# Optimization experiments

Measured on AMD Instinct MI355X. Metric: run time of the kernel, lower is better.

Reference implementation:

```python
import jax, jax.numpy as jnp
import numpy as np

B_SZ, SEQ, D_IN, D_ST, D_OUT = 16, 8192, 128, 128, 128


def setup_inputs() -> dict:
    key = jax.random.key(0)
    ku, ka, kb, kc, kd = jax.random.split(key, 5)
    u = jax.random.normal(ku, (B_SZ, SEQ, D_IN), dtype=jnp.float32)
    # A scaled to spectral radius ~0.9 so the long recurrence stays stable
    A = jax.random.normal(ka, (D_ST, D_ST), dtype=jnp.float32) * (0.9 / np.sqrt(D_ST))
    B = jax.random.normal(kb, (D_ST, D_IN), dtype=jnp.float32) * (1.0 / np.sqrt(D_IN))
    C = jax.random.normal(kc, (D_OUT, D_ST), dtype=jnp.float32) * (1.0 / np.sqrt(D_ST))
    D = jax.random.normal(kd, (D_OUT, D_IN), dtype=jnp.float32) * (1.0 / np.sqrt(D_IN))
    return {"u": u, "A": A, "B": B, "C": C, "D": D}


def reference(u, A, B, C, D):
    # x_t = x_{t-1} A^T + u_t B^T ; y_t = x_t C^T + u_t D^T ; x_0 = 0
    batch = u.shape[0]
    state0 = jnp.zeros((batch, A.shape[0]), dtype=u.dtype)

    def step(state, u_t):  # state: [B, S_dim], u_t: [B, D_in]
        new_state = state @ A.T + u_t @ B.T
        y = new_state @ C.T + u_t @ D.T
        return new_state, y

    u_t_first = jnp.swapaxes(u, 0, 1)  # [SEQ, B, D_in]
    _, ys = jax.lax.scan(step, state0, u_t_first)
    return jnp.swapaxes(ys, 0, 1)  # [B, SEQ, D_out]
```

## Files before the change

kernel.cpp:

```cpp
#include <hip/hip_runtime.h>


#define SEQ 8192
#define BS  16
#define DD  128
#define CL  16
#define NC  512
#define GRP 16
#define NG  32

typedef __bf16 bf16t;
typedef __bf16 bf16x8 __attribute__((ext_vector_type(8)));
typedef __bf16 bf16x4 __attribute__((ext_vector_type(4)));
typedef float  f32x4  __attribute__((ext_vector_type(4)));

#define MFMA(a,b,c) __builtin_amdgcn_mfma_f32_16x16x32_bf16(a,b,c,0,0,0)

__device__ __forceinline__ int swz(int b, int j) { return j ^ ((b & 7) << 3); }

struct Frag  { bf16x8 h[4]; bf16x8 l[4]; };
struct FragH { bf16x8 h[4]; };

__device__ __forceinline__ void load_frag_T(const float* __restrict__ src, int lane, int w, Frag& f) {
    int n  = (w << 4) + (lane & 15);
    int kb = ((lane >> 4) & 3) << 3;
#pragma unroll
    for (int q = 0; q < 4; q++) {
        const float* p = src + n * DD + (q << 5) + kb;
#pragma unroll
        for (int e = 0; e < 8; e++) {
            float v = p[e];
            bf16t hh = (bf16t)v;
            f.h[q][e] = hh;
            f.l[q][e] = (bf16t)(v - (float)hh);
        }
    }
}

__device__ __forceinline__ void load_frag_T_h(const float* __restrict__ src, int lane, int w, FragH& f) {
    int n  = (w << 4) + (lane & 15);
    int kb = ((lane >> 4) & 3) << 3;
#pragma unroll
    for (int q = 0; q < 4; q++) {
        const float* p = src + n * DD + (q << 5) + kb;
#pragma unroll
        for (int e = 0; e < 8; e++) f.h[q][e] = (bf16t)p[e];
    }
}

__device__ __forceinline__ void load_frag_N(const float* __restrict__ src, int lane, int w, Frag& f) {
    int n  = (w << 4) + (lane & 15);
    int kb = ((lane >> 4) & 3) << 3;
#pragma unroll
    for (int q = 0; q < 4; q++) {
#pragma unroll
        for (int e = 0; e < 8; e++) {
            float v = src[((q << 5) + kb + e) * DD + n];
            bf16t hh = (bf16t)v;
            f.h[q][e] = hh;
            f.l[q][e] = (bf16t)(v - (float)hh);
        }
    }
}

__device__ __forceinline__ bf16x8 afrag(const bf16t* __restrict__ X, int lane, int q) {
    int b  = lane & 15;
    int j0 = (q << 5) + (((lane >> 4) & 3) << 3);
    return *(const bf16x8*)(X + b * DD + swz(b, j0));
}

__device__ __forceinline__ void put_state(bf16t* __restrict__ H, bf16t* __restrict__ L,
                                          int lane, int w, f32x4 acc) {
    int n = (w << 4) + (lane & 15);
#pragma unroll
    for (int r = 0; r < 4; r++) {
        int b = (((lane >> 4) & 3) << 2) + r;
        float v = acc[r];
        bf16t hh = (bf16t)v;
        H[b * DD + swz(b, n)] = hh;
        L[b * DD + swz(b, n)] = (bf16t)(v - (float)hh);
    }
}

__device__ __forceinline__ void stage_rows(const float* __restrict__ src, long rs,
                                           bf16t* __restrict__ H, bf16t* __restrict__ L, int tid) {
    int b  = tid >> 5;
    int j0 = (tid & 31) << 2;
    float4 v = *(const float4*)(src + (long)b * rs + j0);
    float vv[4] = { v.x, v.y, v.z, v.w };
    bf16x4 h, l;
#pragma unroll
    for (int e = 0; e < 4; e++) {
        bf16t hh = (bf16t)vv[e];
        h[e] = hh;
        l[e] = (bf16t)(vv[e] - (float)hh);
    }
    *(bf16x4*)(H + b * DD + swz(b, j0)) = h;
    *(bf16x4*)(L + b * DD + swz(b, j0)) = l;
}

__device__ __forceinline__ void write_u_h(bf16t* __restrict__ H, int b_, int j0_, float4 v) {
    float vv[4] = { v.x, v.y, v.z, v.w };
    bf16x4 h;
#pragma unroll
    for (int e = 0; e < 4; e++) h[e] = (bf16t)vv[e];
    *(bf16x4*)(H + b_ * DD + swz(b_, j0_)) = h;
}

__device__ __forceinline__ f32x4 load_accfrag(const float* __restrict__ src, int lane, int w) {
    int n = (w << 4) + (lane & 15);
    f32x4 a;
#pragma unroll
    for (int r = 0; r < 4; r++) {
        int b = (((lane >> 4) & 3) << 2) + r;
        a[r] = src[b * DD + n];
    }
    return a;
}

__device__ __forceinline__ void store_accfrag(float* __restrict__ dst, int lane, int w,
                                              f32x4 a, long rs) {
    int n = (w << 4) + (lane & 15);
#pragma unroll
    for (int r = 0; r < 4; r++) {
        int b = (((lane >> 4) & 3) << 2) + r;
        dst[(long)b * rs + n] = a[r];
    }
}

__global__ __launch_bounds__(128) void k_prepGH(const float* __restrict__ A,
                                                const float* __restrict__ B,
                                                const float* __restrict__ C,
                                                const float* __restrict__ D,
                                                float* __restrict__ Gm, float* __restrict__ Hm) {
    int sel = blockIdx.x >> 7, r = blockIdx.x & 127, j = threadIdx.x;
    const float* R = sel ? B : A;
    float s = 0.f;
#pragma unroll 8
    for (int m = 0; m < 128; m++) s = fmaf(C[r * 128 + m], R[m * 128 + j], s);
    if (sel) Hm[r * 128 + j] = s + D[r * 128 + j];
    else     Gm[r * 128 + j] = s;
}

__global__ __launch_bounds__(512, 4) void k_chunk(const float* __restrict__ u,
                                                  const float* __restrict__ A,
                                                  const float* __restrict__ Bm,
                                                  float* __restrict__ E,
                                                  float* __restrict__ P) {
    __shared__ __align__(16) bf16t Xh[2][BS * DD], Xl[2][BS * DD];
    __shared__ __align__(16) bf16t Uh[2][BS * DD];
    int tid = threadIdx.x, lane = tid & 63, w = tid >> 6;
    bool ident = blockIdx.x < 8;
    int g2 = blockIdx.x, c = blockIdx.x - 8;

    Frag fA; FragH fB;
    load_frag_T(A, lane, w, fA);
    if (!ident) load_frag_T_h(Bm, lane, w, fB);

    for (int i = tid; i < BS * DD; i += 512) {
        int b = i >> 7, j = swz(b, i & 127);
        Xh[0][i] = (bf16t)((ident && j == g2 * 16 + b) ? 1.f : 0.f);
        Xl[0][i] = (bf16t)0.f;
    }
    const float* ubase = u + (long)c * CL * DD;
    int b_ = tid >> 5, j0_ = (tid & 31) << 2;
    if (!ident) {
        float4 v0 = *(const float4*)(ubase + (long)b_ * SEQ * DD + j0_);
        write_u_h(Uh[0], b_, j0_, v0);
    }
    __syncthreads();

    int p = 0;
    f32x4 acc = {0.f, 0.f, 0.f, 0.f};
    for (int i = 0; i < CL; i++) {
        float4 un = {0, 0, 0, 0};
        if (!ident && i + 1 < CL)
            un = *(const float4*)(ubase + (long)b_ * SEQ * DD + (i + 1) * DD + j0_);
        f32x4 ax = {0,0,0,0}, ax2 = {0,0,0,0};
#pragma unroll
        for (int q = 0; q < 4; q++) {
            bf16x8 xh = afrag(Xh[p], lane, q), xl = afrag(Xl[p], lane, q);
            ax  = MFMA(xh, fA.h[q], ax);
            ax2 = MFMA(xl, fA.h[q], ax2);
            ax2 = MFMA(xh, fA.l[q], ax2);
            if (!ident) {
                bf16x8 uh = afrag(Uh[i & 1], lane, q);
                ax = MFMA(uh, fB.h[q], ax);
            }
        }
        acc = ax + ax2;
        if (i + 1 < CL) {
            put_state(Xh[p ^ 1], Xl[p ^ 1], lane, w, acc);
            if (!ident) write_u_h(Uh[(i + 1) & 1], b_, j0_, un);
            __syncthreads();
            p ^= 1;
        }
    }
    if (!ident) store_accfrag(E + (long)c * BS * DD, lane, w, acc, DD);
    else        store_accfrag(P + (long)g2 * 16 * DD, lane, w, acc, DD);
}

__global__ __launch_bounds__(512) void k_group(const float* __restrict__ E,
                                               const float* __restrict__ P,
                                               float* __restrict__ E2,
                                               float* __restrict__ Pg) {
    __shared__ __align__(16) bf16t Xh[2][BS * DD], Xl[2][BS * DD];
    int tid = threadIdx.x, lane = tid & 63, w = tid >> 6;
    bool ident = blockIdx.x >= NG;
    int g2 = blockIdx.x - NG;
    Frag fP;
    load_frag_N(P, lane, w, fP);
    for (int i = tid; i < BS * DD; i += 512) {
        int b = i >> 7, j = swz(b, i & 127);
        Xh[0][i] = (bf16t)((ident && j == g2 * 16 + b) ? 1.f : 0.f);
        Xl[0][i] = (bf16t)0.f;
    }
    __syncthreads();
    int p = 0, g = blockIdx.x;
    f32x4 acc = {0.f, 0.f, 0.f, 0.f};
    for (int r = 0; r < GRP; r++) {
        f32x4 a1 = {0.f,0.f,0.f,0.f}, a2 = {0.f,0.f,0.f,0.f};
        if (!ident) a1 = load_accfrag(E + (long)(g * GRP + r) * BS * DD, lane, w);
#pragma unroll
        for (int q = 0; q < 4; q++) {
            bf16x8 xh = afrag(Xh[p], lane, q), xl = afrag(Xl[p], lane, q);
            a1 = MFMA(xh, fP.h[q], a1);
            a2 = MFMA(xl, fP.h[q], a2);
            a1 = MFMA(xh, fP.l[q], a1);
        }
        acc = a1 + a2;
        if (r + 1 < GRP) {
            put_state(Xh[p ^ 1], Xl[p ^ 1], lane, w, acc);
            __syncthreads();
            p ^= 1;
        }
    }
    if (!ident) store_accfrag(E2 + (long)g * BS * DD, lane, w, acc, DD);
    else        store_accfrag(Pg + (long)g2 * 16 * DD, lane, w, acc, DD);
}

__global__ __launch_bounds__(512) void k_top(const float* __restrict__ E2,
                                             const float* __restrict__ Pg,
                                             float* __restrict__ S2) {
    __shared__ __align__(16) bf16t Xh[2][BS * DD], Xl[2][BS * DD];
    int tid = threadIdx.x, lane = tid & 63, w = tid >> 6;
    Frag fP;
    load_frag_N(Pg, lane, w, fP);
    for (int i = tid; i < BS * DD; i += 512) {
        Xh[0][i] = (bf16t)0.f;
        Xl[0][i] = (bf16t)0.f;
    }
    __syncthreads();
    int p = 0;
    f32x4 T = {0.f, 0.f, 0.f, 0.f};
    f32x4 e2 = load_accfrag(E2, lane, w);
    for (int g = 0; g < NG; g++) {
        store_accfrag(S2 + (long)g * BS * DD, lane, w, T, DD);
        if (g + 1 == NG) break;
        f32x4 e2n = load_accfrag(E2 + (long)(g + 1) * BS * DD, lane, w);
        f32x4 a1 = e2, a2 = {0.f,0.f,0.f,0.f};
#pragma unroll
        for (int q = 0; q < 4; q++) {
            bf16x8 xh = afrag(Xh[p], lane, q), xl = afrag(Xl[p], lane, q);
            a1 = MFMA(xh, fP.h[q], a1);
            a2 = MFMA(xl, fP.h[q], a2);
            a1 = MFMA(xh, fP.l[q], a1);
        }
        T = a1 + a2;
        put_state(Xh[p ^ 1], Xl[p ^ 1], lane, w, T);
        __syncthreads();
        p ^= 1;
        e2 = e2n;
    }
}

__global__ __launch_bounds__(512) void k_fix(float* __restrict__ E,
                                             const float* __restrict__ P,
                                             const float* __restrict__ S2) {
    __shared__ __align__(16) bf16t Xh[2][BS * DD], Xl[2][BS * DD];
    int tid = threadIdx.x, lane = tid & 63, w = tid >> 6;
    int g = blockIdx.x;
    Frag fP;
    load_frag_N(P, lane, w, fP);
    stage_rows(S2 + (long)g * BS * DD, DD, Xh[0], Xl[0], tid);
    f32x4 T = load_accfrag(S2 + (long)g * BS * DD, lane, w);
    __syncthreads();
    int p = 0;
    for (int r = 0; r < GRP; r++) {
        long c = (long)(g * GRP + r) * BS * DD;
        if (r + 1 == GRP) { store_accfrag(E + c, lane, w, T, DD); break; }
        f32x4 a1 = load_accfrag(E + c, lane, w);
        store_accfrag(E + c, lane, w, T, DD);
        f32x4 a2 = {0.f,0.f,0.f,0.f};
#pragma unroll
        for (int q = 0; q < 4; q++) {
            bf16x8 xh = afrag(Xh[p], lane, q), xl = afrag(Xl[p], lane, q);
            a1 = MFMA(xh, fP.h[q], a1);
            a2 = MFMA(xl, fP.h[q], a2);
            a1 = MFMA(xh, fP.l[q], a1);
        }
        T = a1 + a2;
        put_state(Xh[p ^ 1], Xl[p ^ 1], lane, w, T);
        __syncthreads();
        p ^= 1;
    }
}

__global__ __launch_bounds__(512, 4) void k_main(const float* __restrict__ u,
                                                 const float* __restrict__ A,
                                                 const float* __restrict__ Bm,
                                                 const float* __restrict__ Gm,
                                                 const float* __restrict__ Hm,
                                                 const float* __restrict__ S,
                                                 float* __restrict__ out) {
    __shared__ __align__(16) bf16t Xh[2][BS * DD], Xl[2][BS * DD];
    __shared__ __align__(16) bf16t Uh[2][BS * DD];
    int tid = threadIdx.x, lane = tid & 63, w = tid >> 6;
    Frag fA; FragH fB, fG, fH;
    load_frag_T(A, lane, w, fA);
    load_frag_T_h(Bm, lane, w, fB);
    load_frag_T_h(Gm, lane, w, fG);
    load_frag_T_h(Hm, lane, w, fH);
    int c = blockIdx.x;
    const float* ubase = u + (long)c * CL * DD;
    int b_ = tid >> 5, j0_ = (tid & 31) << 2;
    stage_rows(S + (long)c * BS * DD, DD, Xh[0], Xl[0], tid);
    {
        float4 v0 = *(const float4*)(ubase + (long)b_ * SEQ * DD + j0_);
        write_u_h(Uh[0], b_, j0_, v0);
    }
    __syncthreads();
    int p = 0;
    for (int i = 0; i < CL; i++) {
        float4 un = {0, 0, 0, 0};
        if (i + 1 < CL)
            un = *(const float4*)(ubase + (long)b_ * SEQ * DD + (i + 1) * DD + j0_);
        f32x4 ax = {0,0,0,0}, ax2 = {0,0,0,0};
        f32x4 ay = {0,0,0,0}, ay2 = {0,0,0,0};
#pragma unroll
        for (int q = 0; q < 4; q++) {
            bf16x8 xh = afrag(Xh[p], lane, q), xl = afrag(Xl[p], lane, q);
            bf16x8 uh = afrag(Uh[i & 1], lane, q);
            ax  = MFMA(xh, fA.h[q], ax);
            ax  = MFMA(uh, fB.h[q], ax);
            ax2 = MFMA(xl, fA.h[q], ax2);
            ax2 = MFMA(xh, fA.l[q], ax2);
            ay  = MFMA(xh, fG.h[q], ay);
            ay  = MFMA(uh, fH.h[q], ay);
            ay2 = MFMA(xl, fG.h[q], ay2);
        }
        f32x4 xnew = ax + ax2;
        if (i + 1 < CL) {
            put_state(Xh[p ^ 1], Xl[p ^ 1], lane, w, xnew);
            write_u_h(Uh[(i + 1) & 1], b_, j0_, un);
        }
        f32x4 y = ay + ay2;
        store_accfrag(out + ((long)c * CL + i) * DD, lane, w, y, (long)SEQ * DD);
        if (i + 1 < CL) {
            __syncthreads();
            p ^= 1;
        }
    }
}

extern "C" void kernel_launch(void* const* d_in, const int* in_sizes, int n_in,
                              void* d_out, int out_size, void* d_ws, size_t ws_size,
                              hipStream_t stream) {
    (void)in_sizes; (void)n_in; (void)out_size; (void)ws_size;
    const float* u = (const float*)d_in[0];
    const float* A = (const float*)d_in[1];
    const float* B = (const float*)d_in[2];
    const float* C = (const float*)d_in[3];
    const float* D = (const float*)d_in[4];
    float* out = (float*)d_out;
    float* ws  = (float*)d_ws;
    float* Gm = ws;
    float* Hm = Gm + 16384;
    float* P  = Hm + 16384;
    float* Pg = P  + 16384;
    float* E  = Pg + 16384;
    float* E2 = E  + 1048576;
    float* S2 = E2 + 65536;
    dim3 blk(512);
    k_prepGH<<<256, 128, 0, stream>>>(A, B, C, D, Gm, Hm);
    k_chunk<<<NC + 8, blk, 0, stream>>>(u, A, B, E, P);
    k_group<<<NG + 8, blk, 0, stream>>>(E, P, E2, Pg);
    k_top  <<<1,      blk, 0, stream>>>(E2, Pg, S2);
    k_fix  <<<NG,     blk, 0, stream>>>(E, P, S2);
    k_main <<<NC,     blk, 0, stream>>>(u, A, B, Gm, Hm, E, out);
}
```

Before: 137.1 us.

## Replace sequential chunk scan with precomputed A-power kernel matmul and bf16 carries

Precomputes A^2, A^4, A^8, A^16 and the products A^k·B with small MFMA matmul kernels, packing them into one bf16 matrix. Each chunk's end-state contribution then becomes a single parallel GEMM over the 16 inputs instead of a 16-step dependent recurrence. Intermediate carries (E, E2, S2) are stored in bf16, and pass2 stages all chunk inputs into shared memory up front. Barriers use a lighter custom sequence. This adds four small serial prep launches and lowers the precision of the carried states.

Measured after the change: 256.8 us. 1.87x slower.

```diff
diff --git a/kernel.cpp b/kernel.cpp
--- a/kernel.cpp
+++ b/kernel.cpp
@@ -21,6 +21,12 @@
 struct Frag  { bf16x8 h[4]; bf16x8 l[4]; };
 struct FragH { bf16x8 h[4]; };
 
+__device__ __forceinline__ void step_barrier() {
+    asm volatile("s_waitcnt lgkmcnt(0)" ::: "memory");
+    __builtin_amdgcn_s_barrier();
+    __builtin_amdgcn_sched_barrier(0);
+}
+
 __device__ __forceinline__ void load_frag_T(const float* __restrict__ src, int lane, int w, Frag& f) {
     int n  = (w << 4) + (lane & 15);
     int kb = ((lane >> 4) & 3) << 3;
@@ -82,40 +88,36 @@
     }
 }
 
-__device__ __forceinline__ void stage_rows(const float* __restrict__ src, long rs,
-                                           bf16t* __restrict__ H, bf16t* __restrict__ L, int tid) {
+__device__ __forceinline__ void stage_rowsB(const bf16t* __restrict__ src,
+                                            bf16t* __restrict__ H, bf16t* __restrict__ L, int tid) {
     int b  = tid >> 5;
     int j0 = (tid & 31) << 2;
-    float4 v = *(const float4*)(src + (long)b * rs + j0);
-    float vv[4] = { v.x, v.y, v.z, v.w };
-    bf16x4 h, l;
-#pragma unroll
-    for (int e = 0; e < 4; e++) {
-        bf16t hh = (bf16t)vv[e];
-        h[e] = hh;
-        l[e] = (bf16t)(vv[e] - (float)hh);
-    }
-    *(bf16x4*)(H + b * DD + swz(b, j0)) = h;
-    *(bf16x4*)(L + b * DD + swz(b, j0)) = l;
-}
-
-__device__ __forceinline__ void write_u_h(bf16t* __restrict__ H, int b_, int j0_, float4 v) {
-    float vv[4] = { v.x, v.y, v.z, v.w };
-    bf16x4 h;
-#pragma unroll
-    for (int e = 0; e < 4; e++) h[e] = (bf16t)vv[e];
-    *(bf16x4*)(H + b_ * DD + swz(b_, j0_)) = h;
-}
-
-__device__ __forceinline__ f32x4 load_accfrag(const float* __restrict__ src, int lane, int w) {
+    bf16x4 v = *(const bf16x4*)(src + b * DD + j0);
+    *(bf16x4*)(H + b * DD + swz(b, j0)) = v;
+    bf16x4 z;
+    z[0] = z[1] = z[2] = z[3] = (bf16t)0.f;
+    *(bf16x4*)(L + b * DD + swz(b, j0)) = z;
+}
+
+__device__ __forceinline__ f32x4 load_accfragB(const bf16t* __restrict__ src, int lane, int w) {
     int n = (w << 4) + (lane & 15);
     f32x4 a;
 #pragma unroll
     for (int r = 0; r < 4; r++) {
         int b = (((lane >> 4) & 3) << 2) + r;
-        a[r] = src[b * DD + n];
+        a[r] = (float)src[b * DD + n];
     }
     return a;
+}
+
+__device__ __forceinline__ void store_accfragB(bf16t* __restrict__ dst, int lane, int w,
+                                               f32x4 a, long rs) {
+    int n = (w << 4) + (lane & 15);
+#pragma unroll
+    for (int r = 0; r < 4; r++) {
+        int b = (((lane >> 4) & 3) << 2) + r;
+        dst[(long)b * rs + n] = (bf16t)a[r];
+    }
 }
 
 __device__ __forceinline__ void store_accfrag(float* __restrict__ dst, int lane, int w,
@@ -128,99 +130,134 @@
     }
 }
 
-__global__ __launch_bounds__(128) void k_prepGH(const float* __restrict__ A,
-                                                const float* __restrict__ B,
-                                                const float* __restrict__ C,
-                                                const float* __restrict__ D,
-                                                float* __restrict__ Gm, float* __restrict__ Hm) {
-    int sel = blockIdx.x >> 7, r = blockIdx.x & 127, j = threadIdx.x;
-    const float* R = sel ? B : A;
-    float s = 0.f;
-#pragma unroll 8
-    for (int m = 0; m < 128; m++) s = fmaf(C[r * 128 + m], R[m * 128 + j], s);
-    if (sel) Hm[r * 128 + j] = s + D[r * 128 + j];
-    else     Gm[r * 128 + j] = s;
-}
-
-__global__ __launch_bounds__(512, 4) void k_chunk(const float* __restrict__ u,
-                                                  const float* __restrict__ A,
-                                                  const float* __restrict__ Bm,
-                                                  float* __restrict__ E,
-                                                  float* __restrict__ P) {
+__device__ void matmul128(const float* __restrict__ L, const float* __restrict__ R,
+                          const float* __restrict__ Dm, float* __restrict__ outF,
+                          bf16t* __restrict__ pack, int lane, int w) {
+    Frag fB;
+    load_frag_N(R, lane, w, fB);
+    int ln = lane & 15, kq = (lane >> 4) & 3;
+#pragma unroll
+    for (int mt = 0; mt < 8; mt++) {
+        Frag fL;
+        load_frag_T(L, lane, mt, fL);
+        f32x4 ax = {0,0,0,0}, ax2 = {0,0,0,0};
+#pragma unroll
+        for (int q = 0; q < 4; q++) {
+            ax  = MFMA(fL.h[q], fB.h[q], ax);
+            ax2 = MFMA(fL.l[q], fB.h[q], ax2);
+            ax2 = MFMA(fL.h[q], fB.l[q], ax2);
+        }
+        f32x4 a = ax + ax2;
+        int n = (w << 4) + ln;
+#pragma unroll
+        for (int r = 0; r < 4; r++) {
+            int i = mt * 16 + kq * 4 + r;
+            float v = a[r] + (Dm ? Dm[i * DD + n] : 0.f);
+            if (outF) outF[i * DD + n] = v;
+            if (pack) pack[i * DD + n] = (bf16t)v;
+        }
+    }
+}
+
+__global__ __launch_bounds__(512, 2) void k_prepA(const float* __restrict__ A, const float* __restrict__ B,
+                                                  const float* __restrict__ C, const float* __restrict__ D,
+                                                  float* A2, float* Gm, float* Hm, float* S1, bf16t* Kpk) {
+    int tid = threadIdx.x, lane = tid & 63, w = tid >> 6;
+    if      (blockIdx.x == 0) matmul128(A, A, nullptr, A2, nullptr, lane, w);
+    else if (blockIdx.x == 1) matmul128(C, A, nullptr, Gm, nullptr, lane, w);
+    else if (blockIdx.x == 2) matmul128(C, B, D, Hm, nullptr, lane, w);
+    else {
+        matmul128(A, B, nullptr, S1, Kpk + 14 * 16384, lane, w);
+        for (int i = tid; i < 16384; i += 512) Kpk[15 * 16384 + i] = (bf16t)B[i];
+    }
+}
+
+__global__ __launch_bounds__(512, 2) void k_prepB(const float* __restrict__ B, const float* __restrict__ A2,
+                                                  const float* __restrict__ S1,
+                                                  float* A4, float* S2m, float* S3m, bf16t* Kpk) {
+    int lane = threadIdx.x & 63, w = threadIdx.x >> 6;
+    if      (blockIdx.x == 0) matmul128(A2, A2, nullptr, A4,  nullptr,           lane, w);
+    else if (blockIdx.x == 1) matmul128(A2, B,  nullptr, S2m, Kpk + 13 * 16384,  lane, w);
+    else                      matmul128(A2, S1, nullptr, S3m, Kpk + 12 * 16384,  lane, w);
+}
+
+__global__ __launch_bounds__(512, 2) void k_prepC(const float* __restrict__ B, const float* __restrict__ A4,
+                                                  const float* __restrict__ S1, const float* __restrict__ S2m,
+                                                  const float* __restrict__ S3m,
+                                                  float* A8, float* S4m, float* S5m, float* S6m, float* S7m,
+                                                  bf16t* Kpk) {
+    int lane = threadIdx.x & 63, w = threadIdx.x >> 6;
+    if      (blockIdx.x == 0) matmul128(A4, A4,  nullptr, A8,  nullptr,          lane, w);
+    else if (blockIdx.x == 1) matmul128(A4, B,   nullptr, S4m, Kpk + 11 * 16384, lane, w);
+    else if (blockIdx.x == 2) matmul128(A4, S1,  nullptr, S5m, Kpk + 10 * 16384, lane, w);
+    else if (blockIdx.x == 3) matmul128(A4, S2m, nullptr, S6m, Kpk + 9 * 16384,  lane, w);
+    else                      matmul128(A4, S3m, nullptr, S7m, Kpk + 8 * 16384,  lane, w);
+}
+
+__global__ __launch_bounds__(512, 2) void k_prepD(const float* __restrict__ B, const float* __restrict__ A8,
+                                                  const float* __restrict__ S1, const float* __restrict__ S2m,
+                                                  const float* __restrict__ S3m, const float* __restrict__ S4m,
+                                                  const float* __restrict__ S5m, const float* __restrict__ S6m,
+                                                  const float* __restrict__ S7m,
+                                                  float* Pm, bf16t* Kpk) {
+    int lane = threadIdx.x & 63, w = threadIdx.x >> 6;
+    if (blockIdx.x == 0) { matmul128(A8, A8, nullptr, Pm, nullptr, lane, w); return; }
+    const float* Ss[8] = {B, S1, S2m, S3m, S4m, S5m, S6m, S7m};
+    int p = blockIdx.x - 1;
+    matmul128(A8, Ss[p], nullptr, nullptr, Kpk + (7 - p) * 16384, lane, w);
+}
+
+__global__ __launch_bounds__(256, 4) void k_pass1(const float* __restrict__ u,
+                                                  const bf16t* __restrict__ Kpk,
+                                                  bf16t* __restrict__ E) {
+    int tid = threadIdx.x, lane = tid & 63, w = tid >> 6;
+    int b = lane & 15, kg = (lane >> 4) & 3;
+    long c = blockIdx.x;
+    const float* ur = u + (long)b * SEQ * DD + c * CL * DD;
+    f32x4 a0 = {0,0,0,0}, a1 = {0,0,0,0};
+#pragma unroll 4
+    for (int ki = 0; ki < 64; ki++) {
+        const float* p = ur + ki * 32 + kg * 8;
+        float4 v0 = *(const float4*)p;
+        float4 v1 = *(const float4*)(p + 4);
+        bf16x8 uf;
+        uf[0] = (bf16t)v0.x; uf[1] = (bf16t)v0.y; uf[2] = (bf16t)v0.z; uf[3] = (bf16t)v0.w;
+        uf[4] = (bf16t)v1.x; uf[5] = (bf16t)v1.y; uf[6] = (bf16t)v1.z; uf[7] = (bf16t)v1.w;
+        const bf16t* kp = Kpk + (((ki >> 2) * 128 + w * 32 + b) << 7) + (ki & 3) * 32 + kg * 8;
+        bf16x8 k0 = *(const bf16x8*)kp;
+        bf16x8 k1 = *(const bf16x8*)(kp + 16 * 128);
+        a0 = MFMA(uf, k0, a0);
+        a1 = MFMA(uf, k1, a1);
+    }
+    bf16t* eb = E + c * (BS * DD);
+#pragma unroll
+    for (int r = 0; r < 4; r++) {
+        eb[(kg * 4 + r) * DD + w * 32 + b]      = (bf16t)a0[r];
+        eb[(kg * 4 + r) * DD + w * 32 + 16 + b] = (bf16t)a1[r];
+    }
+}
+
+__global__ __launch_bounds__(512, 2) void k_group(const bf16t* __restrict__ E,
+                                                  const float* __restrict__ Pm,
+                                                  bf16t* __restrict__ E2,
+                                                  float* __restrict__ Pg) {
     __shared__ __align__(16) bf16t Xh[2][BS * DD], Xl[2][BS * DD];
-    __shared__ __align__(16) bf16t Uh[2][BS * DD];
-    int tid = threadIdx.x, lane = tid & 63, w = tid >> 6;
-    bool ident = blockIdx.x < 8;
-    int g2 = blockIdx.x, c = blockIdx.x - 8;
-
-    Frag fA; FragH fB;
-    load_frag_T(A, lane, w, fA);
-    if (!ident) load_frag_T_h(Bm, lane, w, fB);
-
+    int tid = threadIdx.x, lane = tid & 63, w = tid >> 6;
+    bool ident = blockIdx.x >= NG;
+    int g2 = blockIdx.x - NG;
+    Frag fP;
+    load_frag_T(Pm, lane, w, fP);
     for (int i = tid; i < BS * DD; i += 512) {
         int b = i >> 7, j = swz(b, i & 127);
         Xh[0][i] = (bf16t)((ident && j == g2 * 16 + b) ? 1.f : 0.f);
         Xl[0][i] = (bf16t)0.f;
     }
-    const float* ubase = u + (long)c * CL * DD;
-    int b_ = tid >> 5, j0_ = (tid & 31) << 2;
-    if (!ident) {
-        float4 v0 = *(const float4*)(ubase + (long)b_ * SEQ * DD + j0_);
-        write_u_h(Uh[0], b_, j0_, v0);
-    }
-    __syncthreads();
-
-    int p = 0;
-    f32x4 acc = {0.f, 0.f, 0.f, 0.f};
-    for (int i = 0; i < CL; i++) {
-        float4 un = {0, 0, 0, 0};
-        if (!ident && i + 1 < CL)
-            un = *(const float4*)(ubase + (long)b_ * SEQ * DD + (i + 1) * DD + j0_);
-        f32x4 ax = {0,0,0,0}, ax2 = {0,0,0,0};
-#pragma unroll
-        for (int q = 0; q < 4; q++) {
-            bf16x8 xh = afrag(Xh[p], lane, q), xl = afrag(Xl[p], lane, q);
-            ax  = MFMA(xh, fA.h[q], ax);
-            ax2 = MFMA(xl, fA.h[q], ax2);
-            ax2 = MFMA(xh, fA.l[q], ax2);
-            if (!ident) {
-                bf16x8 uh = afrag(Uh[i & 1], lane, q);
-                ax = MFMA(uh, fB.h[q], ax);
-            }
-        }
-        acc = ax + ax2;
-        if (i + 1 < CL) {
-            put_state(Xh[p ^ 1], Xl[p ^ 1], lane, w, acc);
-            if (!ident) write_u_h(Uh[(i + 1) & 1], b_, j0_, un);
-            __syncthreads();
-            p ^= 1;
-        }
-    }
-    if (!ident) store_accfrag(E + (long)c * BS * DD, lane, w, acc, DD);
-    else        store_accfrag(P + (long)g2 * 16 * DD, lane, w, acc, DD);
-}
-
-__global__ __launch_bounds__(512) void k_group(const float* __restrict__ E,
-                                               const float* __restrict__ P,
-                                               float* __restrict__ E2,
-                                               float* __restrict__ Pg) {
-    __shared__ __align__(16) bf16t Xh[2][BS * DD], Xl[2][BS * DD];
-    int tid = threadIdx.x, lane = tid & 63, w = tid >> 6;
-    bool ident = blockIdx.x >= NG;
-    int g2 = blockIdx.x - NG;
-    Frag fP;
-    load_frag_N(P, lane, w, fP);
-    for (int i = tid; i < BS * DD; i += 512) {
-        int b = i >> 7, j = swz(b, i & 127);
-        Xh[0][i] = (bf16t)((ident && j == g2 * 16 + b) ? 1.f : 0.f);
-        Xl[0][i] = (bf16t)0.f;
-    }
     __syncthreads();
     int p = 0, g = blockIdx.x;
-    f32x4 acc = {0.f, 0.f, 0.f, 0.f};
+    f32x4 acc = {0,0,0,0};
     for (int r = 0; r < GRP; r++) {
-        f32x4 a1 = {0.f,0.f,0.f,0.f}, a2 = {0.f,0.f,0.f,0.f};
-        if (!ident) a1 = load_accfrag(E + (long)(g * GRP + r) * BS * DD, lane, w);
+        f32x4 a1 = {0,0,0,0}, a2 = {0,0,0,0};
+        if (!ident) a1 = load_accfragB(E + (long)(g * GRP + r) * BS * DD, lane, w);
 #pragma unroll
         for (int q = 0; q < 4; q++) {
             bf16x8 xh = afrag(Xh[p], lane, q), xl = afrag(Xl[p], lane, q);
@@ -231,17 +268,17 @@
         acc = a1 + a2;
         if (r + 1 < GRP) {
             put_state(Xh[p ^ 1], Xl[p ^ 1], lane, w, acc);
-            __syncthreads();
+            step_barrier();
             p ^= 1;
         }
     }
-    if (!ident) store_accfrag(E2 + (long)g * BS * DD, lane, w, acc, DD);
+    if (!ident) store_accfragB(E2 + (long)g * BS * DD, lane, w, acc, DD);
     else        store_accfrag(Pg + (long)g2 * 16 * DD, lane, w, acc, DD);
 }
 
-__global__ __launch_bounds__(512) void k_top(const float* __restrict__ E2,
-                                             const float* __restrict__ Pg,
-                                             float* __restrict__ S2) {
+__global__ __launch_bounds__(512, 2) void k_top(const bf16t* __restrict__ E2,
+                                                const float* __restrict__ Pg,
+                                                bf16t* __restrict__ S2) {
     __shared__ __align__(16) bf16t Xh[2][BS * DD], Xl[2][BS * DD];
     int tid = threadIdx.x, lane = tid & 63, w = tid >> 6;
     Frag fP;
@@ -252,13 +289,11 @@
     }
     __syncthreads();
     int p = 0;
-    f32x4 T = {0.f, 0.f, 0.f, 0.f};
-    f32x4 e2 = load_accfrag(E2, lane, w);
+    f32x4 T = {0,0,0,0};
     for (int g = 0; g < NG; g++) {
-        store_accfrag(S2 + (long)g * BS * DD, lane, w, T, DD);
+        store_accfragB(S2 + (long)g * BS * DD, lane, w, T, DD);
         if (g + 1 == NG) break;
-        f32x4 e2n = load_accfrag(E2 + (long)(g + 1) * BS * DD, lane, w);
-        f32x4 a1 = e2, a2 = {0.f,0.f,0.f,0.f};
+        f32x4 a1 = load_accfragB(E2 + (long)g * BS * DD, lane, w), a2 = {0,0,0,0};
 #pragma unroll
         for (int q = 0; q < 4; q++) {
             bf16x8 xh = afrag(Xh[p], lane, q), xl = afrag(Xl[p], lane, q);
@@ -268,30 +303,29 @@
         }
         T = a1 + a2;
         put_state(Xh[p ^ 1], Xl[p ^ 1], lane, w, T);
-        __syncthreads();
+        step_barrier();
         p ^= 1;
-        e2 = e2n;
-    }
-}
-
-__global__ __launch_bounds__(512) void k_fix(float* __restrict__ E,
-                                             const float* __restrict__ P,
-                                             const float* __restrict__ S2) {
+    }
+}
+
+__global__ __launch_bounds__(512, 2) void k_fix(bf16t* __restrict__ E,
+                                                const float* __restrict__ Pm,
+                                                const bf16t* __restrict__ S2) {
     __shared__ __align__(16) bf16t Xh[2][BS * DD], Xl[2][BS * DD];
     int tid = threadIdx.x, lane = tid & 63, w = tid >> 6;
     int g = blockIdx.x;
     Frag fP;
-    load_frag_N(P, lane, w, fP);
-    stage_rows(S2 + (long)g * BS * DD, DD, Xh[0], Xl[0], tid);
-    f32x4 T = load_accfrag(S2 + (long)g * BS * DD, lane, w);
+    load_frag_T(Pm, lane, w, fP);
+    stage_rowsB(S2 + (long)g * BS * DD, Xh[0], Xl[0], tid);
+    f32x4 T = load_accfragB(S2 + (long)g * BS * DD, lane, w);
     __syncthreads();
     int p = 0;
     for (int r = 0; r < GRP; r++) {
-        long c = (long)(g * GRP + r) * BS * DD;
-        if (r + 1 == GRP) { store_accfrag(E + c, lane, w, T, DD); break; }
-        f32x4 a1 = load_accfrag(E + c, lane, w);
-        store_accfrag(E + c, lane, w, T, DD);
-        f32x4 a2 = {0.f,0.f,0.f,0.f};
+        long cc = (long)(g * GRP + r) * BS * DD;
+        f32x4 a1 = load_accfragB(E + cc, lane, w);
+        store_accfragB(E + cc, lane, w, T, DD);
+        if (r + 1 == GRP) break;
+        f32x4 a2 = {0,0,0,0};
 #pragma unroll
         for (int q = 0; q < 4; q++) {
             bf16x8 xh = afrag(Xh[p], lane, q), xl = afrag(Xl[p], lane, q);
@@ -301,64 +335,66 @@
         }
         T = a1 + a2;
         put_state(Xh[p ^ 1], Xl[p ^ 1], lane, w, T);
-        __syncthreads();
+        step_barrier();
         p ^= 1;
     }
 }
 
-__global__ __launch_bounds__(512, 4) void k_main(const float* __restrict__ u,
-                                                 const float* __restrict__ A,
-                                                 const float* __restrict__ Bm,
-                                                 const float* __restrict__ Gm,
-                                                 const float* __restrict__ Hm,
-                                                 const float* __restrict__ S,
-                                                 float* __restrict__ out) {
+__global__ __launch_bounds__(512, 2) void k_pass2(const float* __restrict__ u,
+                                                  const float* __restrict__ Am,
+                                                  const float* __restrict__ Bm,
+                                                  const float* __restrict__ Gm,
+                                                  const float* __restrict__ Hm,
+                                                  const bf16t* __restrict__ S,
+                                                  float* __restrict__ out) {
+    __shared__ __align__(16) bf16t Uh[CL * BS * DD];
     __shared__ __align__(16) bf16t Xh[2][BS * DD], Xl[2][BS * DD];
-    __shared__ __align__(16) bf16t Uh[2][BS * DD];
-    int tid = threadIdx.x, lane = tid & 63, w = tid >> 6;
+    int tid = threadIdx.x, lane = tid & 63, w = tid >> 6;
+    long c = blockIdx.x;
     Frag fA; FragH fB, fG, fH;
-    load_frag_T(A, lane, w, fA);
+    load_frag_T(Am, lane, w, fA);
     load_frag_T_h(Bm, lane, w, fB);
     load_frag_T_h(Gm, lane, w, fG);
     load_frag_T_h(Hm, lane, w, fH);
-    int c = blockIdx.x;
-    const float* ubase = u + (long)c * CL * DD;
-    int b_ = tid >> 5, j0_ = (tid & 31) << 2;
-    stage_rows(S + (long)c * BS * DD, DD, Xh[0], Xl[0], tid);
+    stage_rowsB(S + c * (BS * DD), Xh[0], Xl[0], tid);
     {
-        float4 v0 = *(const float4*)(ubase + (long)b_ * SEQ * DD + j0_);
-        write_u_h(Uh[0], b_, j0_, v0);
-    }
-    __syncthreads();
-    int p = 0;
-    for (int i = 0; i < CL; i++) {
-        float4 un = {0, 0, 0, 0};
-        if (i + 1 < CL)
-            un = *(const float4*)(ubase + (long)b_ * SEQ * DD + (i + 1) * DD + j0_);
-        f32x4 ax = {0,0,0,0}, ax2 = {0,0,0,0};
-        f32x4 ay = {0,0,0,0}, ay2 = {0,0,0,0};
+        int b_ = tid >> 5, j0_ = (tid & 31) << 2;
+        const float* ub = u + (long)b_ * SEQ * DD + c * CL * DD + j0_;
+        bf16t* uw = Uh + b_ * DD + swz(b_, j0_);
+#pragma unroll
+        for (int j = 0; j < CL; j++) {
+            float4 v = *(const float4*)(ub + j * DD);
+            bf16x4 h;
+            h[0] = (bf16t)v.x; h[1] = (bf16t)v.y; h[2] = (bf16t)v.z; h[3] = (bf16t)v.w;
+            *(bf16x4*)(uw + j * (BS * DD)) = h;
+        }
+    }
+    step_barrier();
+#pragma unroll
+    for (int t = 0; t < CL; t++) {
+        f32x4 ax = {0,0,0,0}, axb = {0,0,0,0}, ax2 = {0,0,0,0}, ax2b = {0,0,0,0};
+        f32x4 ay = {0,0,0,0}, ayb = {0,0,0,0};
 #pragma unroll
         for (int q = 0; q < 4; q++) {
-            bf16x8 xh = afrag(Xh[p], lane, q), xl = afrag(Xl[p], lane, q);
-            bf16x8 uh = afrag(Uh[i & 1], lane, q);
-            ax  = MFMA(xh, fA.h[q], ax);
-            ax  = MFMA(uh, fB.h[q], ax);
-            ax2 = MFMA(xl, fA.h[q], ax2);
-            ax2 = MFMA(xh, fA.l[q], ax2);
+            bf16x8 xh = afrag(Xh[t & 1], lane, q);
+            bf16x8 xl = afrag(Xl[t & 1], lane, q);
+            bf16x8 uh = afrag(Uh + t * (BS * DD), lane, q);
+            if (t + 1 < CL) {
+                ax   = MFMA(xh, fA.h[q], ax);
+                axb  = MFMA(uh, fB.h[q], axb);
+                ax2  = MFMA(xl, fA.h[q], ax2);
+                ax2b = MFMA(xh, fA.l[q], ax2b);
+            }
             ay  = MFMA(xh, fG.h[q], ay);
-            ay  = MFMA(uh, fH.h[q], ay);
-            ay2 = MFMA(xl, fG.h[q], ay2);
-        }
-        f32x4 xnew = ax + ax2;
-        if (i + 1 < CL) {
-            put_state(Xh[p ^ 1], Xl[p ^ 1], lane, w, xnew);
-            write_u_h(Uh[(i + 1) & 1], b_, j0_, un);
-        }
-        f32x4 y = ay + ay2;
-        store_accfrag(out + ((long)c * CL + i) * DD, lane, w, y, (long)SEQ * DD);
-        if (i + 1 < CL) {
-            __syncthreads();
-            p ^= 1;
+            ay  = MFMA(xl, fG.h[q], ay);
+            ayb = MFMA(uh, fH.h[q], ayb);
+        }
+        f32x4 y = ay + ayb;
+        store_accfrag(out + (c * CL + t) * DD, lane, w, y, (long)SEQ * DD);
+        if (t + 1 < CL) {
+            f32x4 xnew = (ax + axb) + (ax2 + ax2b);
+            put_state(Xh[(t + 1) & 1], Xl[(t + 1) & 1], lane, w, xnew);
+            step_barrier();
         }
     }
 }
@@ -373,19 +409,33 @@
     const float* C = (const float*)d_in[3];
     const float* D = (const float*)d_in[4];
     float* out = (float*)d_out;
-    float* ws  = (float*)d_ws;
-    float* Gm = ws;
-    float* Hm = Gm + 16384;
-    float* P  = Hm + 16384;
-    float* Pg = P  + 16384;
-    float* E  = Pg + 16384;
-    float* E2 = E  + 1048576;
-    float* S2 = E2 + 65536;
-    dim3 blk(512);
-    k_prepGH<<<256, 128, 0, stream>>>(A, B, C, D, Gm, Hm);
-    k_chunk<<<NC + 8, blk, 0, stream>>>(u, A, B, E, P);
-    k_group<<<NG + 8, blk, 0, stream>>>(E, P, E2, Pg);
-    k_top  <<<1,      blk, 0, stream>>>(E2, Pg, S2);
-    k_fix  <<<NG,     blk, 0, stream>>>(E, P, S2);
-    k_main <<<NC,     blk, 0, stream>>>(u, A, B, Gm, Hm, E, out);
-}
+    float* fp  = (float*)d_ws;
+    float* A2  = fp;             fp += 16384;
+    float* A4  = fp;             fp += 16384;
+    float* A8  = fp;             fp += 16384;
+    float* Pm  = fp;             fp += 16384;
+    float* Pg  = fp;             fp += 16384;
+    float* Gm  = fp;             fp += 16384;
+    float* Hm  = fp;             fp += 16384;
+    float* S1  = fp;             fp += 16384;
+    float* S2m = fp;             fp += 16384;
+    float* S3m = fp;             fp += 16384;
+    float* S4m = fp;             fp += 16384;
+    float* S5m = fp;             fp += 16384;
+    float* S6m = fp;             fp += 16384;
+    float* S7m = fp;             fp += 16384;
+    bf16t* E   = (bf16t*)fp;     fp += 524288;
+    bf16t* E2  = (bf16t*)fp;     fp += 32768;
+    bf16t* S2b = (bf16t*)fp;     fp += 32768;
+    bf16t* Kpk = (bf16t*)fp;     fp += 131072;
+
+    k_prepA<<<4, 512, 0, stream>>>(A, B, C, D, A2, Gm, Hm, S1, Kpk);
+    k_prepB<<<3, 512, 0, stream>>>(B, A2, S1, A4, S2m, S3m, Kpk);
+    k_prepC<<<5, 512, 0, stream>>>(B, A4, S1, S2m, S3m, A8, S4m, S5m, S6m, S7m, Kpk);
+    k_prepD<<<9, 512, 0, stream>>>(B, A8, S1, S2m, S3m, S4m, S5m, S6m, S7m, Pm, Kpk);
+    k_pass1<<<NC, 256, 0, stream>>>(u, Kpk, E);
+    k_group<<<NG + 8, 512, 0, stream>>>(E, Pm, E2, Pg);
+    k_top  <<<1, 512, 0, stream>>>(E2, Pg, S2b);
+    k_fix  <<<NG, 512, 0, stream>>>(E, Pm, S2b);
+    k_pass2<<<NC, 512, 0, stream>>>(u, A, B, Gm, Hm, E, out);
+}
```
